# Performance work log

Hardware: AMD Instinct MI355X
Metric: run time of the kernel (lower is better)

## Reference

```python
import jax, jax.numpy as jnp
import numpy as np
from jax import lax

B, LS, LT, C, H, GRID = 32, 256, 128, 768, 12, 16
KEEP_RATIO = 0.7

def _ln(x, w, b):
    mu = x.mean(-1, keepdims=True)
    var = ((x - mu) ** 2).mean(-1, keepdims=True)
    return (x - mu) / jnp.sqrt(var + 1e-5) * w + b

def _gelu(x):
    return jax.nn.gelu(x, approximate=False)

def setup_inputs() -> dict:
    key = jax.random.key(0)
    ks = jax.random.split(key, 16)
    w = lambda k, s: jax.random.normal(k, s, jnp.float32) * 0.02
    N = LT + LS
    return {
        'x': jax.random.normal(ks[0], (B, N, C), jnp.float32),
        'global_index_template': jax.random.randint(ks[1], (B, LT), 0, LT).astype(jnp.int32),
        'global_index_search': jax.random.randint(ks[2], (B, LS), 0, LS).astype(jnp.int32),
        'learn_template_mask': jax.random.uniform(ks[3], (2, B, LT // 2), jnp.float32),
        'ln1_w': jnp.ones((C,), jnp.float32), 'ln1_b': jnp.zeros((C,), jnp.float32),
        'qkv_w': w(ks[4], (C, 3 * C)),
        'proj_w': w(ks[5], (C, C)), 'proj_b': jnp.zeros((C,), jnp.float32),
        'ln2_w': jnp.ones((C,), jnp.float32), 'ln2_b': jnp.zeros((C,), jnp.float32),
        'fc1_w': w(ks[6], (C, 4 * C)), 'fc1_b': jnp.zeros((4 * C,), jnp.float32),
        'fc2_w': w(ks[7], (4 * C, C)), 'fc2_b': jnp.zeros((C,), jnp.float32),
        'd1_w': w(ks[8], (3 * C, 768)), 'd1_b': jnp.zeros((768,), jnp.float32),
        'd2_w': w(ks[9], (768, 384)), 'd2_b': jnp.zeros((384,), jnp.float32),
        'd3_w': w(ks[10], (384, 192)), 'd3_b': jnp.zeros((192,), jnp.float32),
        'd4_w': w(ks[11], (192, 1)), 'd4_b': jnp.zeros((1,), jnp.float32),
    }

def reference(x, global_index_template, global_index_search, learn_template_mask,
              ln1_w, ln1_b, qkv_w, proj_w, proj_b, ln2_w, ln2_b,
              fc1_w, fc1_b, fc2_w, fc2_b,
              d1_w, d1_b, d2_w, d2_b, d3_w, d3_b, d4_w, d4_b):
    bs = x.shape[0]
    lt = global_index_template.shape[1]
    ls = global_index_search.shape[1]
    half = lt // 2
    # --- roimax target representations ---
    init_rep = jnp.max(x[:, :half] * learn_template_mask[0][..., None], axis=1, keepdims=True)   # [B,1,C]
    dyn_rep = jnp.max(x[:, half:lt] * learn_template_mask[1][..., None], axis=1, keepdims=True)  # [B,1,C]
    feat = jnp.concatenate([x[:, -ls:],
                            jnp.broadcast_to(init_rep, (bs, ls, C)),
                            jnp.broadcast_to(dyn_rep, (bs, ls, C))], axis=-1)  # [B,ls,3C]
    h = _gelu(feat @ d1_w + d1_b)
    h = _gelu(h @ d2_w + d2_b)
    h = _gelu(h @ d3_w + d3_b)
    pred = h @ d4_w + d4_b                      # [B,ls,1]
    probs = jax.nn.sigmoid(pred)                # foreground probabilities
    # --- 3x3 region-sum conv and argmax center ---
    grid = probs.reshape(bs, 1, GRID, GRID)
    kern = jnp.ones((1, 1, 3, 3), grid.dtype)
    filt = lax.conv_general_dilated(grid, kern, (1, 1), 'SAME',
                                    dimension_numbers=('NCHW', 'OIHW', 'NCHW'))
    max_idx = jnp.argmax(filt.reshape(bs, -1), axis=1)
    cx, cy = max_idx // GRID, max_idx % GRID
    gx = jnp.arange(GRID)[None, :, None]
    gy = jnp.arange(GRID)[None, None, :]
    win = lambda r: ((jnp.abs(gx - cx[:, None, None]) <= r) &
                     (jnp.abs(gy - cy[:, None, None]) <= r)).reshape(bs, GRID * GRID)
    mask7, mask11 = win(3), win(5)
    foreground = (probs > 0.5).astype(jnp.int32)          # [B,ls,1]
    selected_fg = foreground * mask7[..., None].astype(jnp.int32)
    # --- candidate elimination: keep all tokens inside 11x11 window first, then top prob ---
    lens_keep = int(np.ceil(KEEP_RATIO * ls))
    p_out = jnp.where(mask11, jnp.inf, probs[..., 0])     # [B,ls]
    order = jnp.argsort(-p_out, axis=1)                   # stable descending
    topk_idx, non_topk = order[:, :lens_keep], order[:, lens_keep:]
    keep_index = jnp.take_along_axis(global_index_search, topk_idx, axis=1)
    removed_index = jnp.take_along_axis(global_index_search, non_topk, axis=1)
    xs = jnp.take_along_axis(x[:, lt:], topk_idx[..., None], axis=1)  # [B,lens_keep,C]
    xnew = jnp.concatenate([x[:, :lt], xs], axis=1)       # [B, lt+lens_keep, C]
    sf = jnp.take_along_axis(selected_fg, topk_idx[..., None], axis=1)[..., 0]
    decision = jax.nn.one_hot(sf, 2, dtype=x.dtype)       # scatter_(2, sf, 1)
    search_policy = jnp.concatenate([jnp.zeros((bs, lens_keep, 2), x.dtype), decision], -1)
    template_policy = jnp.zeros((bs, half, 4), x.dtype).at[:, :, 0].set(1.0)
    dynamic_policy = jnp.zeros((bs, half, 4), x.dtype).at[:, :, 1].set(1.0)
    P = jnp.concatenate([template_policy, dynamic_policy, search_policy], axis=1)
    key_bg = P[:, :, 2] > 0.5    # background search tokens -> masked as attention keys
    # --- attention ---
    n = xnew.shape[1]
    dh = C // H
    hn = _ln(xnew, ln1_w, ln1_b)
    qkv = (hn @ qkv_w).reshape(bs, n, 3, H, dh).transpose(2, 0, 3, 1, 4)
    q, k, v = qkv[0], qkv[1], qkv[2]
    scores = jnp.einsum('bhnd,bhmd->bhnm', q, k) * dh ** -0.5
    scores = jnp.where(key_bg[:, None, None, :], -1e9, scores)
    attn = jax.nn.softmax(scores, axis=-1)
    out = jnp.einsum('bhnm,bhmd->bhnd', attn, v).transpose(0, 2, 1, 3).reshape(bs, n, C)
    xnew = xnew + (out @ proj_w + proj_b)
    m = _ln(xnew, ln2_w, ln2_b)
    xout = xnew + (_gelu(m @ fc1_w + fc1_b) @ fc2_w + fc2_b)
    return (xout, keep_index, removed_index, attn)
```

## Files before the change

### kernel.cpp

```cpp
#include <hip/hip_runtime.h>
#include <hip/hip_bf16.h>
#include <math.h>

#define BB 32
#define LSN 256
#define LTN 128
#define CCH 768
#define NHH 12
#define NTOK 384
#define NKEEP 180
#define NREM 76
#define NNEW 308
#define MS 8192
#define MN 9856

typedef unsigned short u16;
typedef __attribute__((ext_vector_type(8))) short s8v;
typedef __attribute__((ext_vector_type(4))) float f4v;

__device__ __forceinline__ u16 f2bf(float x) {
    union { __hip_bfloat16 b; u16 u; } c; c.b = __float2bfloat16(x); return c.u;
}
__device__ __forceinline__ float bf2f(u16 u) {
    return __uint_as_float(((unsigned)u) << 16);
}
__device__ __forceinline__ void gl_lds16(const u16* g, u16* l) {
    __builtin_amdgcn_global_load_lds((const __attribute__((address_space(1))) unsigned*)g,
                                     (__attribute__((address_space(3))) unsigned*)l, 16, 0, 0);
}
__device__ __forceinline__ int xcd_swz(int lin, int nwg) {
    int q = nwg >> 3, r = nwg & 7;
    int xcd = lin & 7, idx = lin >> 3;
    return (xcd < r ? xcd * (q + 1) : r * (q + 1) + (xcd - r) * q) + idx;
}

__global__ void k_fail(float* o, float v) { o[0] = v; }

__global__ void k_reps(const float* __restrict__ x, const float* __restrict__ mask,
                       float* __restrict__ rep0, float* __restrict__ rep1) {
    int b = blockIdx.x, t = threadIdx.x;
    float m0[3] = {-INFINITY, -INFINITY, -INFINITY};
    float m1[3] = {-INFINITY, -INFINITY, -INFINITY};
    for (int i = 0; i < 64; ++i) {
        float mk0 = mask[b * 64 + i];
        float mk1 = mask[BB * 64 + b * 64 + i];
        const float* r0 = x + (size_t)(b * NTOK + i) * CCH;
        const float* r1 = x + (size_t)(b * NTOK + 64 + i) * CCH;
#pragma unroll
        for (int j = 0; j < 3; ++j) {
            m0[j] = fmaxf(m0[j], r0[t + 256 * j] * mk0);
            m1[j] = fmaxf(m1[j], r1[t + 256 * j] * mk1);
        }
    }
#pragma unroll
    for (int j = 0; j < 3; ++j) {
        rep0[b * CCH + t + 256 * j] = m0[j];
        rep1[b * CCH + t + 256 * j] = m1[j];
    }
}

__device__ __forceinline__ float gelu_np(float v) {
    float t = v / 1.4142135623730951f;
    float ef = (float)erf((double)t);
    return 0.5f * v * (1.0f + ef);
}

template<int ROWMAP>
__global__ __launch_bounds__(256) void gemm_exact(const float* __restrict__ A,
                                                  const float* __restrict__ rep0, const float* __restrict__ rep1,
                                                  const float* __restrict__ W, const float* __restrict__ bias,
                                                  float* __restrict__ out, int N, int K) {
    __shared__ float As[32 * 64];
    __shared__ float Bs[32 * 64];
    int t = threadIdx.x;
    int tx = t & 15, ty = t >> 4;
    int bm = blockIdx.y * 64, bn = blockIdx.x * 64;
    int b = bm >> 8;
    float acc[4][4] = {};

    int arow = t >> 2;
    int ak = (t & 3) * 4;
    int asw = arow ^ ((ak & 4) << 2);
    size_t aoff;
    if (ROWMAP) aoff = (size_t)(b * NTOK + LTN + ((bm + arow) & 255)) * CCH;
    else        aoff = (size_t)(bm + arow) * K;

    int bkr = t >> 4, bc = (t & 15) * 4;

#define LOADA(kg) (ROWMAP ? (((kg) < CCH) ? *(const float4*)&A[aoff + (kg)] \
                    : (((kg) < 2*CCH) ? *(const float4*)&rep0[b*CCH + (kg) - CCH] \
                                      : *(const float4*)&rep1[b*CCH + (kg) - 2*CCH])) \
                   : *(const float4*)&A[aoff + (kg)])

    int nt = K >> 5;
    float4 ra0 = LOADA(ak), ra1 = LOADA(16 + ak);
    float4 rb0 = *(const float4*)&W[(size_t)bkr * N + bn + bc];
    float4 rb1 = *(const float4*)&W[(size_t)(16 + bkr) * N + bn + bc];

    for (int tile = 0; tile < nt; ++tile) {
        __syncthreads();
        As[(ak + 0) * 64 + asw] = ra0.x; As[(ak + 1) * 64 + asw] = ra0.y;
        As[(ak + 2) * 64 + asw] = ra0.z; As[(ak + 3) * 64 + asw] = ra0.w;
        As[(16 + ak + 0) * 64 + asw] = ra1.x; As[(16 + ak + 1) * 64 + asw] = ra1.y;
        As[(16 + ak + 2) * 64 + asw] = ra1.z; As[(16 + ak + 3) * 64 + asw] = ra1.w;
        *(float4*)&Bs[t * 4] = rb0;
        *(float4*)&Bs[1024 + t * 4] = rb1;
        if (tile + 1 < nt) {
            int k0 = (tile + 1) << 5;
            ra0 = LOADA(k0 + ak); ra1 = LOADA(k0 + 16 + ak);
            rb0 = *(const float4*)&W[(size_t)(k0 + bkr) * N + bn + bc];
            rb1 = *(const float4*)&W[(size_t)(k0 + 16 + bkr) * N + bn + bc];
        }
        __syncthreads();
#pragma unroll
        for (int k = 0; k < 32; ++k) {
            float a[4], bv[4];
            *(float4*)&a[0]  = *(const float4*)&As[k * 64 + ((ty * 4) ^ ((k & 4) << 2))];
            *(float4*)&bv[0] = *(const float4*)&Bs[k * 64 + tx * 4];
#pragma unroll
            for (int i = 0; i < 4; ++i)
#pragma unroll
                for (int j = 0; j < 4; ++j) acc[i][j] = fmaf(a[i], bv[j], acc[i][j]);
        }
    }
#undef LOADA
#pragma unroll
    for (int i = 0; i < 4; ++i) {
        int m = bm + ty * 4 + i;
        float4 o;
        o.x = gelu_np(acc[i][0] + bias[bn + tx * 4 + 0]);
        o.y = gelu_np(acc[i][1] + bias[bn + tx * 4 + 1]);
        o.z = gelu_np(acc[i][2] + bias[bn + tx * 4 + 2]);
        o.w = gelu_np(acc[i][3] + bias[bn + tx * 4 + 3]);
        *(float4*)&out[(size_t)m * N + bn + tx * 4] = o;
    }
}

__global__ void k_d4(const float* __restrict__ h3, const float* __restrict__ w4,
                     const float* __restrict__ b4, float* __restrict__ probs) {
    int m = blockIdx.x * 256 + threadIdx.x;
    if (m >= MS) return;
    float acc = 0.f;
    for (int k = 0; k < 192; ++k) acc = fmaf(h3[(size_t)m * 192 + k], w4[k], acc);
    float pred = acc + b4[0];
    float ef = (float)exp(-(double)pred);
    probs[m] = 1.0f / (1.0f + ef);
}

__global__ void k_selsort(const float* __restrict__ probs, const int* __restrict__ gis,
                          float* __restrict__ keep_out, float* __restrict__ rem_out,
                          int* __restrict__ topk, int* __restrict__ keybg) {
    int b = blockIdx.x, t = threadIdx.x;
    __shared__ float pr[256];
    __shared__ double ft[256];
    __shared__ int cxy[2];
    __shared__ float pout[256];
    __shared__ int sf[256];
    __shared__ int ord[256];
    pr[t] = probs[b * 256 + t];
    __syncthreads();
    int X = t >> 4, Y = t & 15;
    double s = 0.0;
    for (int dx = -1; dx <= 1; ++dx)
        for (int dy = -1; dy <= 1; ++dy) {
            int xx = X + dx, yy = Y + dy;
            if (xx >= 0 && xx < 16 && yy >= 0 && yy < 16) s += (double)pr[xx * 16 + yy];
        }
    ft[t] = s;
    __syncthreads();
    if (t == 0) {
        double best = ft[0]; int bi = 0;
        for (int i = 1; i < 256; ++i) if (ft[i] > best) { best = ft[i]; bi = i; }
        cxy[0] = bi >> 4; cxy[1] = bi & 15;
    }
    __syncthreads();
    int cx = cxy[0], cy = cxy[1];
    int ax = X - cx; if (ax < 0) ax = -ax;
    int ay = Y - cy; if (ay < 0) ay = -ay;
    bool m7  = (ax <= 3) && (ay <= 3);
    bool m11 = (ax <= 5) && (ay <= 5);
    int fg = (pr[t] > 0.5f) ? 1 : 0;
    sf[t] = m7 ? fg : 0;
    pout[t] = m11 ? INFINITY : pr[t];
    __syncthreads();
    float pi = pout[t];
    int rank = 0;
    for (int j = 0; j < 256; ++j) {
        float pj = pout[j];
        rank += (pj > pi) || (pj == pi && j < t);
    }
    ord[rank] = t;
    __syncthreads();
    int idx = ord[t];
    int g = gis[b * 256 + idx];
    if (t < NKEEP) {
        keep_out[b * NKEEP + t] = (float)g;
        topk[b * NKEEP + t] = idx;
        keybg[b * NNEW + LTN + t] = (sf[idx] == 0) ? 1 : 0;
    } else {
        rem_out[b * NREM + (t - NKEEP)] = (float)g;
    }
    if (t < LTN) keybg[b * NNEW + t] = 0;
}

__global__ void k_xnew_ln(const float* __restrict__ x, const int* __restrict__ topk,
                          const float* __restrict__ w, const float* __restrict__ b,
                          float* __restrict__ out_x, u16* __restrict__ hn) {
    int row = blockIdx.x, t = threadIdx.x;
    int bb = row / NNEW, r = row - bb * NNEW;
    int src = (r < LTN) ? r : (LTN + topk[bb * NKEEP + (r - LTN)]);
    const float* p = x + (size_t)(bb * NTOK + src) * CCH;
    __shared__ float s1[256], s2[256];
    float v[3]; float a0 = 0.f, a1 = 0.f;
#pragma unroll
    for (int i = 0; i < 3; ++i) { v[i] = p[t + 256 * i]; a0 += v[i]; a1 += v[i] * v[i]; }
#pragma unroll
    for (int i = 0; i < 3; ++i) out_x[(size_t)row * CCH + t + 256 * i] = v[i];
    s1[t] = a0; s2[t] = a1;
    __syncthreads();
    for (int off = 128; off > 0; off >>= 1) {
        if (t < off) { s1[t] += s1[t + off]; s2[t] += s2[t + off]; }
        __syncthreads();
    }
    float mu = s1[0] * (1.0f / CCH);
    float var = s2[0] * (1.0f / CCH) - mu * mu;
    float rstd = rsqrtf(var + 1e-5f);
#pragma unroll
    for (int i = 0; i < 3; ++i) {
        int c = t + 256 * i;
        hn[(size_t)row * CCH + c] = f2bf((v[i] - mu) * rstd * w[c] + b[c]);
    }
}


__global__ void k_ln_bf(const float* __restrict__ in, const float* __restrict__ w, const float* __restrict__ b,
                        u16* __restrict__ out) {
    int row = blockIdx.x, t = threadIdx.x;
    __shared__ float s1[256], s2[256];
    const float* p = in + (size_t)row * CCH;
    float v[3]; float a0 = 0.f, a1 = 0.f;
#pragma unroll
    for (int i = 0; i < 3; ++i) { v[i] = p[t + 256 * i]; a0 += v[i]; a1 += v[i] * v[i]; }
    s1[t] = a0; s2[t] = a1;
    __syncthreads();
    for (int off = 128; off > 0; off >>= 1) {
        if (t < off) { s1[t] += s1[t + off]; s2[t] += s2[t + off]; }
        __syncthreads();
    }
    float mu = s1[0] * (1.0f / CCH);
    float var = s2[0] * (1.0f / CCH) - mu * mu;
    float rstd = rsqrtf(var + 1e-5f);
#pragma unroll
    for (int i = 0; i < 3; ++i) {
        int c = t + 256 * i;
        out[(size_t)row * CCH + c] = f2bf((v[i] - mu) * rstd * w[c] + b[c]);
    }
}

__global__ void k_prep(const float* __restrict__ qkvw, const float* __restrict__ projw,
                       const float* __restrict__ fc1w, const float* __restrict__ fc2w,
                       u16* __restrict__ qkvwT, u16* __restrict__ projwT,
                       u16* __restrict__ fc1wT, u16* __restrict__ fc2wT) {
    int id = blockIdx.x;
    int t = threadIdx.x;
    const float* W; u16* Wt; int K, N, tile;
    if (id < 1728)      { W = qkvw;  Wt = qkvwT;  K = 768;  N = 2304; tile = id; }
    else if (id < 2304) { W = projw; Wt = projwT; K = 768;  N = 768;  tile = id - 1728; }
    else if (id < 4608) { W = fc1w;  Wt = fc1wT;  K = 768;  N = 3072; tile = id - 2304; }
    else                { W = fc2w;  Wt = fc2wT;  K = 3072; N = 768;  tile = id - 4608; }
    int kt = K >> 5;
    int k0 = (tile % kt) * 32, n0 = (tile / kt) * 32;
    __shared__ float tilebuf[32][33];
    int tx = t & 31, ty = t >> 5;
    for (int i = ty; i < 32; i += 8) tilebuf[i][tx] = W[(size_t)(k0 + i) * N + n0 + tx];
    __syncthreads();
    for (int i = ty; i < 32; i += 8) Wt[(size_t)(n0 + i) * K + k0 + tx] = f2bf(tilebuf[tx][i]);
}

template<int MODE>
__global__ __launch_bounds__(256) void gemm_bf16(const u16* __restrict__ A, const u16* __restrict__ Bt,
                                                 const float* __restrict__ bias, const float* __restrict__ res,
                                                 float* __restrict__ outf, u16* __restrict__ outb,
                                                 u16* __restrict__ vbuf, int N, int K) {
    __shared__ u16 sm[2][2][4096];
    int t = threadIdx.x, lane = t & 63, wid = t >> 6;
    int nwg = gridDim.x * gridDim.y;
    int lin = blockIdx.y * gridDim.x + blockIdx.x;
    int T = xcd_swz(lin, nwg);
    int bx = T % gridDim.x, by = T / gridDim.x;
    int bm = by * 128, bn = bx * 128;
    const u16* pA[2]; const u16* pB[2];
#pragma unroll
    for (int i = 0; i < 2; ++i) {
        int L = wid * 128 + i * 64 + lane;
        int line = L >> 3, sp = L & 7, sl = sp ^ (line & 7);
        int r = (line << 1) | (sl >> 2), k0 = (sl & 3) << 3;
        pA[i] = A + (size_t)(bm + r) * K + k0;
        pB[i] = Bt + (size_t)(bn + r) * K + k0;
    }
    int wr = wid >> 1, wc = wid & 1;
    int l15 = lane & 15, l4 = lane >> 4;
    int rA = wr * 64 + l15, rB = wc * 64 + l15;
    int offA = (rA >> 1) * 128 + (((((rA & 1) << 2) | l4)) ^ ((rA >> 1) & 7)) * 16;
    int offB = (rB >> 1) * 128 + (((((rB & 1) << 2) | l4)) ^ ((rB >> 1) & 7)) * 16;
    f4v zero = {0.f, 0.f, 0.f, 0.f};
    f4v acc[4][4];
#pragma unroll
    for (int i = 0; i < 4; ++i)
#pragma unroll
        for (int j = 0; j < 4; ++j) acc[i][j] = zero;

#define STAGE_G(buf, kt) { \
    u16* da = &sm[buf][0][wid * 1024]; u16* db = &sm[buf][1][wid * 1024]; \
    gl_lds16(pA[0] + (kt) * 32, da); \
    gl_lds16(pA[1] + (kt) * 32, da + 512); \
    gl_lds16(pB[0] + (kt) * 32, db); \
    gl_lds16(pB[1] + (kt) * 32, db + 512); \
}
    int nk = K >> 5;
    STAGE_G(0, 0);
    __syncthreads();
    for (int kt = 0; kt < nk; ++kt) {
        int cur = kt & 1;
        if (kt + 1 < nk) STAGE_G(cur ^ 1, kt + 1);
        const char* bA = (const char*)&sm[cur][0][0];
        const char* bBp = (const char*)&sm[cur][1][0];
        s8v a[4], b[4];
#pragma unroll
        for (int i = 0; i < 4; ++i) {
            a[i] = *(const s8v*)(bA + offA + i * 1024);
            b[i] = *(const s8v*)(bBp + offB + i * 1024);
        }
#pragma unroll
        for (int mf = 0; mf < 4; ++mf)
#pragma unroll
            for (int nf = 0; nf < 4; ++nf)
                acc[mf][nf] = __builtin_amdgcn_mfma_f32_16x16x32_bf16(a[mf], b[nf], acc[mf][nf], 0, 0, 0);
        __syncthreads();
    }
#undef STAGE_G
#pragma unroll
    for (int mf = 0; mf < 4; ++mf)
#pragma unroll
        for (int nf = 0; nf < 4; ++nf)
#pragma unroll
            for (int j = 0; j < 4; ++j) {
                int row = bm + wr * 64 + mf * 16 + l4 * 4 + j;
                int col = bn + wc * 64 + nf * 16 + l15;
                float v = acc[mf][nf][j];
                if (MODE == 0) {
                    if (col < 1536) {
                        if (col < 768) v *= 0.125f;
                        outb[(size_t)row * 1536 + col] = f2bf(v);
                    } else {
                        vbuf[(size_t)row * 768 + (col - 1536)] = f2bf(v);
                    }
                } else if (MODE == 1) {
                    outf[(size_t)row * N + col] = v + bias[col] + res[(size_t)row * N + col];
                } else {
                    float g = v + bias[col];
                    g = 0.5f * g * (1.0f + erff(g * 0.70710678f));
                    outb[(size_t)row * N + col] = f2bf(g);
                }
            }
}

__global__ __launch_bounds__(256) void k_attn2(const u16* __restrict__ qkvQK, const u16* __restrict__ vbuf,
                                               const int* __restrict__ keybg,
                                               float* __restrict__ attn_out, u16* __restrict__ ctx) {
    __shared__ __align__(16) char smem[98560];
    u16* Qs = (u16*)smem;
    u16* Ks = (u16*)(smem + 9216);
    u16* Ss = (u16*)(smem + 55296);
    int* kb = (int*)(smem + 97280);
    float* OT = (float*)Ss;
    u16* Vts = Ks;

    int nwg = gridDim.x * gridDim.y;
    int lin = blockIdx.y * gridDim.x + blockIdx.x;
    int T = xcd_swz(lin, nwg);
    int bh = T / 5;
    int q0 = (T - bh * 5) * 64;
    int b = bh / NHH, h = bh % NHH;
    int nq = NNEW - q0; if (nq > 64) nq = 64;
    int t = threadIdx.x, lane = t & 63, wid = t >> 6;
    int l15 = lane & 15, l4 = lane >> 4;
    s8v z = {0, 0, 0, 0, 0, 0, 0, 0};

    {
        int r = t >> 2, c = (t & 3) * 16;
        u16* dst = Qs + r * 72 + c;
        if (r < nq) {
            const u16* src = qkvQK + (size_t)(b * NNEW + q0 + r) * 1536 + h * 64 + c;
            *(s8v*)dst = *(const s8v*)src;
            *(s8v*)(dst + 8) = *(const s8v*)(src + 8);
        } else { *(s8v*)dst = z; *(s8v*)(dst + 8) = z; }
    }
    for (int it = 0; it < 5; ++it) {
        int r = it * 64 + (t >> 2), c = (t & 3) * 16;
        u16* dst = Ks + r * 72 + c;
        if (r < NNEW) {
            const u16* src = qkvQK + (size_t)(b * NNEW + r) * 1536 + 768 + h * 64 + c;
            *(s8v*)dst = *(const s8v*)src;
            *(s8v*)(dst + 8) = *(const s8v*)(src + 8);
        } else { *(s8v*)dst = z; *(s8v*)(dst + 8) = z; }
    }
    for (int i = t; i < 320; i += 256) kb[i] = (i < NNEW) ? keybg[b * NNEW + i] : 1;
    __syncthreads();

    f4v zero = {0.f, 0.f, 0.f, 0.f};
    f4v acc[4][5];
#pragma unroll
    for (int i = 0; i < 4; ++i)
#pragma unroll
        for (int j = 0; j < 5; ++j) acc[i][j] = zero;
#pragma unroll
    for (int ks = 0; ks < 2; ++ks) {
        s8v a[4], bf[5];
#pragma unroll
        for (int mf = 0; mf < 4; ++mf) a[mf] = *(const s8v*)(Qs + (mf * 16 + l15) * 72 + ks * 32 + l4 * 8);
#pragma unroll
        for (int nf = 0; nf < 5; ++nf) bf[nf] = *(const s8v*)(Ks + (wid * 80 + nf * 16 + l15) * 72 + ks * 32 + l4 * 8);
#pragma unroll
        for (int mf = 0; mf < 4; ++mf)
#pragma unroll
            for (int nf = 0; nf < 5; ++nf)
                acc[mf][nf] = __builtin_amdgcn_mfma_f32_16x16x32_bf16(a[mf], bf[nf], acc[mf][nf], 0, 0, 0);
    }
#pragma unroll
    for (int nf = 0; nf < 5; ++nf) {
        int n = wid * 80 + nf * 16 + l15;
        int msk = kb[n];
#pragma unroll
        for (int mf = 0; mf < 4; ++mf)
#pragma unroll
            for (int j = 0; j < 4; ++j) {
                int q = mf * 16 + l4 * 4 + j;
                float v = msk ? -1e9f : acc[mf][nf][j];
                Ss[q * 328 + n] = f2bf(v);
            }
    }
    __syncthreads();

    {
        for (int it = 0; it < 5; ++it) {
            int tok = it * 64 + (t >> 2);
            int d0 = (t & 3) * 16;
            if (tok < NNEW) {
                const u16* src = vbuf + (size_t)(b * NNEW + tok) * 768 + h * 64 + d0;
                s8v v0 = *(const s8v*)src;
                s8v v1 = *(const s8v*)(src + 8);
#pragma unroll
                for (int j = 0; j < 8; ++j) Vts[(d0 + j) * 328 + tok] = (u16)v0[j];
#pragma unroll
                for (int j = 0; j < 8; ++j) Vts[(d0 + 8 + j) * 328 + tok] = (u16)v1[j];
            } else if (tok < 320) {
#pragma unroll
                for (int j = 0; j < 16; ++j) Vts[(d0 + j) * 328 + tok] = 0;
            }
        }
    }
    {
        int q = t >> 2, j4 = t & 3;
        u16* row = Ss + q * 328 + j4 * 80;
        float mx = -3e38f;
#pragma unroll
        for (int i = 0; i < 10; ++i) {
            s8v vv = *(const s8v*)(row + i * 8);
#pragma unroll
            for (int e = 0; e < 8; ++e) mx = fmaxf(mx, bf2f((u16)vv[e]));
        }
        mx = fmaxf(mx, __shfl_xor(mx, 1));
        mx = fmaxf(mx, __shfl_xor(mx, 2));
        float sum = 0.f;
#pragma unroll
        for (int i = 0; i < 10; ++i) {
            s8v vv = *(const s8v*)(row + i * 8);
            s8v ov;
#pragma unroll
            for (int e = 0; e < 8; ++e) {
                float ex = expf(bf2f((u16)vv[e]) - mx);
                sum += ex;
                ov[e] = (short)f2bf(ex);
            }
            *(s8v*)(row + i * 8) = ov;
        }
        sum += __shfl_xor(sum, 1);
        sum += __shfl_xor(sum, 2);
        float inv = 1.0f / sum;
#pragma unroll
        for (int i = 0; i < 10; ++i) {
            s8v vv = *(const s8v*)(row + i * 8);
            s8v ov;
            float pf[8];
#pragma unroll
            for (int e = 0; e < 8; ++e) {
                float p = bf2f((u16)vv[e]) * inv;
                pf[e] = p;
                ov[e] = (short)f2bf(p);
            }
            *(s8v*)(row + i * 8) = ov;
            if (q < nq) {
                int n0 = j4 * 80 + i * 8;
                float* dst = attn_out + ((size_t)bh * NNEW + q0 + q) * NNEW + n0;
#pragma unroll
                for (int e = 0; e < 8; ++e) if (n0 + e < NNEW) dst[e] = pf[e];
            }
        }
    }
    __syncthreads();

    f4v o[4];
#pragma unroll
    for (int i = 0; i < 4; ++i) o[i] = zero;
    int dblk = wid * 16;
#pragma unroll
    for (int ks = 0; ks < 10; ++ks) {
        s8v av = *(const s8v*)(Vts + (dblk + l15) * 328 + ks * 32 + l4 * 8);
#pragma unroll
        for (int nf = 0; nf < 4; ++nf) {
            s8v pv = *(const s8v*)(Ss + (nf * 16 + l15) * 328 + ks * 32 + l4 * 8);
            o[nf] = __builtin_amdgcn_mfma_f32_16x16x32_bf16(av, pv, o[nf], 0, 0, 0);
        }
    }
    __syncthreads();
#pragma unroll
    for (int nf = 0; nf < 4; ++nf)
#pragma unroll
        for (int j = 0; j < 4; ++j)
            OT[(dblk + l4 * 4 + j) * 65 + nf * 16 + l15] = o[nf][j];
    __syncthreads();
    {
        int q = t >> 2, c = t & 3;
        if (q < nq) {
            u16 buf[16];
#pragma unroll
            for (int i = 0; i < 16; ++i) buf[i] = f2bf(OT[(c * 16 + i) * 65 + q]);
            u16* dst = ctx + (size_t)(b * NNEW + q0 + q) * CCH + h * 64 + c * 16;
            *(s8v*)dst = *(const s8v*)&buf[0];
            *(s8v*)(dst + 8) = *(const s8v*)&buf[8];
        }
    }
}

extern "C" void kernel_launch(void* const* d_in, const int* in_sizes, int n_in,
                              void* d_out, int out_size, void* d_ws, size_t ws_size,
                              hipStream_t stream) {
    const float* x     = (const float*)d_in[0];
    const int*   gis   = (const int*)d_in[2];
    const float* mask  = (const float*)d_in[3];
    const float* ln1w  = (const float*)d_in[4];
    const float* ln1b  = (const float*)d_in[5];
    const float* qkvw  = (const float*)d_in[6];
    const float* projw = (const float*)d_in[7];
    const float* projb = (const float*)d_in[8];
    const float* ln2w  = (const float*)d_in[9];
    const float* ln2b  = (const float*)d_in[10];
    const float* fc1w  = (const float*)d_in[11];
    const float* fc1b  = (const float*)d_in[12];
    const float* fc2w  = (const float*)d_in[13];
    const float* fc2b  = (const float*)d_in[14];
    const float* d1w   = (const float*)d_in[15];
    const float* d1b   = (const float*)d_in[16];
    const float* d2w   = (const float*)d_in[17];
    const float* d2b   = (const float*)d_in[18];
    const float* d3w   = (const float*)d_in[19];
    const float* d3b   = (const float*)d_in[20];
    const float* d4w   = (const float*)d_in[21];
    const float* d4b   = (const float*)d_in[22];

    float* out_x    = (float*)d_out;
    float* out_keep = out_x + 7569408;
    float* out_rem  = out_keep + 5760;
    float* out_attn = out_rem + 2432;

    char* ws = (char*)d_ws;
    u16* hn_bf  = (u16*)(ws);
    u16* qkvQK  = (u16*)(ws + 15138816);
    u16* vbuf   = (u16*)(ws + 45416448);
    u16* fc1_bf = (u16*)(ws);
    u16* ctx_bf = (u16*)(ws + 60751872);
    u16* qkvwT  = (u16*)(ws + 75890688);
    u16* projwT = (u16*)(ws + 79429632);
    u16* fc1wT  = (u16*)(ws + 80609280);
    u16* fc2wT  = (u16*)(ws + 85327872);
    char* misc  = ws + 90046464;
    float* rep0  = (float*)(misc + 0 * 262144);
    float* rep1  = (float*)(misc + 1 * 262144);
    float* probs = (float*)(misc + 2 * 262144);
    int*   topk  = (int*)(misc + 5 * 262144);
    int*   keybg = (int*)(misc + 6 * 262144);
    size_t required = 90046464ull + 7ull * 262144ull;
    if (ws_size < required) {
        k_fail<<<1, 1, 0, stream>>>((float*)d_out, (float)(ws_size / 1048576.0));
        return;
    }

    float* h1 = (float*)out_attn;
    float* h2 = h1 + 8192 * 768;
    float* h3 = h2 + 8192 * 384;

    k_prep<<<6912, 256, 0, stream>>>(qkvw, projw, fc1w, fc2w, qkvwT, projwT, fc1wT, fc2wT);

    k_reps<<<BB, 256, 0, stream>>>(x, mask, rep0, rep1);
    gemm_exact<1><<<dim3(12, 128), 256, 0, stream>>>(x, rep0, rep1, d1w, d1b, h1, 768, 2304);
    gemm_exact<0><<<dim3(6, 128), 256, 0, stream>>>(h1, nullptr, nullptr, d2w, d2b, h2, 384, 768);
    gemm_exact<0><<<dim3(3, 128), 256, 0, stream>>>(h2, nullptr, nullptr, d3w, d3b, h3, 192, 384);
    k_d4<<<MS / 256, 256, 0, stream>>>(h3, d4w, d4b, probs);
    k_selsort<<<BB, 256, 0, stream>>>(probs, gis, out_keep, out_rem, topk, keybg);
    k_xnew_ln<<<MN, 256, 0, stream>>>(x, topk, ln1w, ln1b, out_x, hn_bf);

    gemm_bf16<0><<<dim3(18, 77), 256, 0, stream>>>(hn_bf, qkvwT, nullptr, nullptr, nullptr, qkvQK, vbuf, 2304, 768);
    k_attn2<<<dim3(5, 384), 256, 0, stream>>>(qkvQK, vbuf, keybg, out_attn, ctx_bf);
    gemm_bf16<1><<<dim3(6, 77), 256, 0, stream>>>(ctx_bf, projwT, projb, out_x, out_x, nullptr, nullptr, 768, 768);
    k_ln_bf<<<MN, 256, 0, stream>>>(out_x, ln2w, ln2b, ctx_bf);
    gemm_bf16<2><<<dim3(24, 77), 256, 0, stream>>>(ctx_bf, fc1wT, fc1b, nullptr, nullptr, fc1_bf, nullptr, 3072, 768);
    gemm_bf16<1><<<dim3(6, 77), 256, 0, stream>>>(fc1_bf, fc2wT, fc2b, out_x, out_x, nullptr, nullptr, 768, 3072);
}
```

Before: 985.4 us.

## Pack FMAs in exact FP32 GEMM, swizzle tiles across XCDs, fuse d4 into sort

The FP32 decision-MLP GEMM now computes its inner product on two-wide float vectors so the compiler can emit packed FMA instructions, and remaps workgroup IDs with an XCD-aware swizzle to improve L2 locality. The d4 projection plus sigmoid is folded into the selection/sort kernel, which removes one launch and the round trip through the probs buffer. In exchange, the d4 dot products now run on only 32 blocks, so each thread reads a 192-float row serially with less parallelism. Each packed FMA is still a single rounding per element, so results should not change.

```diff
diff --git a/kernel.cpp b/kernel.cpp
--- a/kernel.cpp
+++ b/kernel.cpp
@@ -17,6 +17,7 @@
 typedef unsigned short u16;
 typedef __attribute__((ext_vector_type(8))) short s8v;
 typedef __attribute__((ext_vector_type(4))) float f4v;
+typedef __attribute__((ext_vector_type(2))) float f2v;
 
 __device__ __forceinline__ u16 f2bf(float x) {
     union { __hip_bfloat16 b; u16 u; } c; c.b = __float2bfloat16(x); return c.u;
@@ -74,9 +75,14 @@
     __shared__ float Bs[32 * 64];
     int t = threadIdx.x;
     int tx = t & 15, ty = t >> 4;
-    int bm = blockIdx.y * 64, bn = blockIdx.x * 64;
+    int nbx = N >> 6;
+    int nwg = nbx * gridDim.y;
+    int lin = blockIdx.y * nbx + blockIdx.x;
+    int T = xcd_swz(lin, nwg);
+    int bxs = T % nbx, bys = T / nbx;
+    int bm = bys * 64, bn = bxs * 64;
     int b = bm >> 8;
-    float acc[4][4] = {};
+    f2v acc2[4][2] = {};
 
     int arow = t >> 2;
     int ak = (t & 3) * 4;
@@ -117,10 +123,13 @@
             float a[4], bv[4];
             *(float4*)&a[0]  = *(const float4*)&As[k * 64 + ((ty * 4) ^ ((k & 4) << 2))];
             *(float4*)&bv[0] = *(const float4*)&Bs[k * 64 + tx * 4];
-#pragma unroll
-            for (int i = 0; i < 4; ++i)
-#pragma unroll
-                for (int j = 0; j < 4; ++j) acc[i][j] = fmaf(a[i], bv[j], acc[i][j]);
+            f2v b0 = {bv[0], bv[1]}, b1 = {bv[2], bv[3]};
+#pragma unroll
+            for (int i = 0; i < 4; ++i) {
+                f2v av = {a[i], a[i]};
+                acc2[i][0] = __builtin_elementwise_fma(av, b0, acc2[i][0]);
+                acc2[i][1] = __builtin_elementwise_fma(av, b1, acc2[i][1]);
+            }
         }
     }
 #undef LOADA
@@ -128,28 +137,18 @@
     for (int i = 0; i < 4; ++i) {
         int m = bm + ty * 4 + i;
         float4 o;
-        o.x = gelu_np(acc[i][0] + bias[bn + tx * 4 + 0]);
-        o.y = gelu_np(acc[i][1] + bias[bn + tx * 4 + 1]);
-        o.z = gelu_np(acc[i][2] + bias[bn + tx * 4 + 2]);
-        o.w = gelu_np(acc[i][3] + bias[bn + tx * 4 + 3]);
+        o.x = gelu_np(acc2[i][0][0] + bias[bn + tx * 4 + 0]);
+        o.y = gelu_np(acc2[i][0][1] + bias[bn + tx * 4 + 1]);
+        o.z = gelu_np(acc2[i][1][0] + bias[bn + tx * 4 + 2]);
+        o.w = gelu_np(acc2[i][1][1] + bias[bn + tx * 4 + 3]);
         *(float4*)&out[(size_t)m * N + bn + tx * 4] = o;
     }
 }
 
-__global__ void k_d4(const float* __restrict__ h3, const float* __restrict__ w4,
-                     const float* __restrict__ b4, float* __restrict__ probs) {
-    int m = blockIdx.x * 256 + threadIdx.x;
-    if (m >= MS) return;
-    float acc = 0.f;
-    for (int k = 0; k < 192; ++k) acc = fmaf(h3[(size_t)m * 192 + k], w4[k], acc);
-    float pred = acc + b4[0];
-    float ef = (float)exp(-(double)pred);
-    probs[m] = 1.0f / (1.0f + ef);
-}
-
-__global__ void k_selsort(const float* __restrict__ probs, const int* __restrict__ gis,
-                          float* __restrict__ keep_out, float* __restrict__ rem_out,
-                          int* __restrict__ topk, int* __restrict__ keybg) {
+__global__ void k_d4sort(const float* __restrict__ h3, const float* __restrict__ w4,
+                         const float* __restrict__ b4, const int* __restrict__ gis,
+                         float* __restrict__ keep_out, float* __restrict__ rem_out,
+                         int* __restrict__ topk, int* __restrict__ keybg) {
     int b = blockIdx.x, t = threadIdx.x;
     __shared__ float pr[256];
     __shared__ double ft[256];
@@ -157,7 +156,14 @@
     __shared__ float pout[256];
     __shared__ int sf[256];
     __shared__ int ord[256];
-    pr[t] = probs[b * 256 + t];
+    {
+        int m = b * 256 + t;
+        float acc = 0.f;
+        for (int k = 0; k < 192; ++k) acc = fmaf(h3[(size_t)m * 192 + k], w4[k], acc);
+        float pred = acc + b4[0];
+        float ef = (float)exp(-(double)pred);
+        pr[t] = 1.0f / (1.0f + ef);
+    }
     __syncthreads();
     int X = t >> 4, Y = t & 15;
     double s = 0.0;
@@ -587,7 +593,6 @@
     char* misc  = ws + 90046464;
     float* rep0  = (float*)(misc + 0 * 262144);
     float* rep1  = (float*)(misc + 1 * 262144);
-    float* probs = (float*)(misc + 2 * 262144);
     int*   topk  = (int*)(misc + 5 * 262144);
     int*   keybg = (int*)(misc + 6 * 262144);
     size_t required = 90046464ull + 7ull * 262144ull;
@@ -606,8 +611,7 @@
     gemm_exact<1><<<dim3(12, 128), 256, 0, stream>>>(x, rep0, rep1, d1w, d1b, h1, 768, 2304);
     gemm_exact<0><<<dim3(6, 128), 256, 0, stream>>>(h1, nullptr, nullptr, d2w, d2b, h2, 384, 768);
     gemm_exact<0><<<dim3(3, 128), 256, 0, stream>>>(h2, nullptr, nullptr, d3w, d3b, h3, 192, 384);
-    k_d4<<<MS / 256, 256, 0, stream>>>(h3, d4w, d4b, probs);
-    k_selsort<<<BB, 256, 0, stream>>>(probs, gis, out_keep, out_rem, topk, keybg);
+    k_d4sort<<<BB, 256, 0, stream>>>(h3, d4w, d4b, gis, out_keep, out_rem, topk, keybg);
     k_xnew_ln<<<MN, 256, 0, stream>>>(x, topk, ln1w, ln1b, out_x, hn_bf);
 
     gemm_bf16<0><<<dim3(18, 77), 256, 0, stream>>>(hn_bf, qkvwT, nullptr, nullptr, nullptr, qkvQK, vbuf, 2304, 768);
```

New measurement: 991.1 us. About the same (+0.6%).
